# Performance work log

Hardware: AMD Instinct MI355X
Metric: run time of the kernel (lower is better)

Reference implementation:

```python
import jax, jax.numpy as jnp
import numpy as np
from jax import lax

WIDTH = 3.0
SIGMA = 1.0
REDIST_ITERS = 10
B, N = 64, 512  # grid is N x N


def _coords(H, W):
    ys = jnp.arange(H, dtype=jnp.float32)[:, None] * jnp.ones((1, W), jnp.float32)
    xs = jnp.arange(W, dtype=jnp.float32)[None, :] * jnp.ones((H, 1), jnp.float32)
    return xs, ys  # x = column, y = row


def _bilinear_splat(values, xf, yf, H, W):
    """Scatter-add `values` at continuous (xf, yf) with bilinear weights."""
    x0 = jnp.floor(xf)
    y0 = jnp.floor(yf)
    fx = xf - x0
    fy = yf - y0
    x0i = x0.astype(jnp.int32)
    y0i = y0.astype(jnp.int32)
    grid = jnp.zeros((H, W), values.dtype)
    for dx, dy in ((0, 0), (1, 0), (0, 1), (1, 1)):
        xi = x0i + dx
        yi = y0i + dy
        w = (fx if dx else 1.0 - fx) * (fy if dy else 1.0 - fy)
        valid = (xi >= 0) & (xi < W) & (yi >= 0) & (yi < H)
        xi_c = jnp.clip(xi, 0, W - 1)
        yi_c = jnp.clip(yi, 0, H - 1)
        grid = grid.at[yi_c, xi_c].add(jnp.where(valid, w * values, 0.0))
    return grid


def _push_one(rho, p0, p1):
    """Differentiable push via bilinear splat. rho: (H, W) image convention."""
    H, W = rho.shape
    xs, ys = _coords(H, W)
    d = p1 - p0
    L = jnp.sqrt(jnp.sum(d * d) + 1e-12)
    u = d / L                              # unit push direction (x, y)
    n = jnp.stack([-u[1], u[0]])           # unit normal
    rx = xs - p0[0]
    ry = ys - p0[1]
    s = rx * u[0] + ry * u[1]              # along-push coordinate
    t = rx * n[0] + ry * n[1]              # perpendicular coordinate
    sig = jax.nn.sigmoid
    mask = sig((WIDTH - jnp.abs(t)) / SIGMA) * sig(s / SIGMA) * sig((L - s) / SIGMA)
    moved = rho * mask
    disp = jnp.maximum(L - s, 0.0)         # push swept mass to the tool front
    xf = (xs + disp * u[0]).ravel()
    yf = (ys + disp * u[1]).ravel()
    splat = _bilinear_splat(moved.ravel(), xf, yf, H, W)
    return rho * (1.0 - mask) + splat, mask


def _redistribute_one(rho, u):
    """Diffuse occupancy excess (>1) one voxel forward along u, iteratively."""
    H, W = rho.shape
    xs, ys = _coords(H, W)
    xf = (xs + u[0]).ravel()
    yf = (ys + u[1]).ravel()

    def step(r, _):
        exc = jax.nn.relu(r - 1.0)
        shifted = _bilinear_splat(exc.ravel(), xf, yf, H, W)
        return r - exc + shifted, None

    rho, _ = lax.scan(step, rho, None, length=REDIST_ITERS)
    return rho


def setup_inputs() -> dict:
    key = jax.random.key(0)
    k1, k2, k3 = jax.random.split(key, 3)
    occ = jax.random.uniform(k1, (B, N, N), dtype=jnp.float32)
    action_start = jax.random.uniform(k2, (B, 2), dtype=jnp.float32) * (N - 1)
    action_end = jax.random.uniform(k3, (B, 2), dtype=jnp.float32) * (N - 1)
    return {"occ": occ, "action_start": action_start, "action_end": action_end}


def reference(occ, action_start, action_end):
    rho = jnp.transpose(occ, (0, 2, 1))          # (B, Nx, Ny) -> (B, H=y, W=x)
    p0 = action_start[:, :2]
    p1 = action_end[:, :2]
    rho_new, _ = jax.vmap(_push_one)(rho, p0, p1)
    d = p1 - p0
    d_norm = jnp.sqrt(jnp.sum(d * d, axis=-1))
    u = d / jnp.maximum(d_norm, 1e-6)[:, None]
    rho_red = jax.vmap(_redistribute_one)(rho_new, u)
    rho_out = jnp.where((d_norm > 1e-6)[:, None, None], rho_red, rho_new)
    return jnp.transpose(rho_out, (0, 2, 1))
```

## Files before the change

### kernel.cpp

```cpp
#include <hip/hip_runtime.h>

#define NN   512
#define NN2  (NN * NN)
#define BB   64
#define ITERS 10
#define WM   40
#define WWIN (WM * WM)
#define SBLK 16
#define NSPLAT (BB * SBLK)
#define GPT  4
#define NSTREAM 2048
#define FTPB 512

#define RD   64
#define RST  69
#define RTPB 1024

__device__ __forceinline__ float sigf(float x) { return 1.0f / (1.0f + __expf(-x)); }

__device__ __forceinline__ float maskf(float s, float t, float L) {
    if (fabsf(t) > 30.f || s < -30.f || s > L + 30.f) return 0.f;
    return sigf(3.f - fabsf(t)) * sigf(s) * sigf(L - s);
}

__device__ __forceinline__ float base_elem2(float o, float s, float t, float L) {
    float m = maskf(s, t, L);
    return (s >= L) ? o : o * (1.f - m);
}

__global__ void __launch_bounds__(FTPB) fused_kernel(
        const float* __restrict__ occ,
        const float* __restrict__ as_,
        const float* __restrict__ ae_,
        float* __restrict__ ws,
        float* __restrict__ out) {
    __shared__ float win[WWIN];
    const int bid = blockIdx.x;
    const int tid = threadIdx.x;

    if (bid < NSPLAT) {
        const int b  = bid >> 4;
        const int qb = bid & (SBLK - 1);

        const float p0x = as_[2 * b], p0y = as_[2 * b + 1];
        const float p1x = ae_[2 * b], p1y = ae_[2 * b + 1];
        const float dx = p1x - p0x, dy = p1y - p0y;
        const float L  = sqrtf(dx * dx + dy * dy + 1e-12f);
        const float u0 = dx / L, u1 = dy / L;
        const float au0 = fabsf(u0), au1 = fabsf(u1);
        const int wx0 = (int)floorf(p1x - 16.f * au1) - 2;
        const int wy0 = (int)floorf(p1y - 16.f * au0) - 2;
        const bool degen = (dx == 0.f && dy == 0.f);

        for (int k = tid; k < WWIN; k += FTPB) win[k] = 0.f;
        __syncthreads();

        if (!degen) {
            const float* ob = occ + ((size_t)b << 18);
            const bool caseA = (au0 >= au1);
            const int wave = tid >> 6;
            const int lane = tid & 63;

            #pragma unroll
            for (int k2 = 0; k2 < 4; ++k2) {
                const int a = qb + 16 * (wave + 8 * k2);
                const float fa = (float)a;
                float lo, hi;
                bool skip = false;
                if (caseA) {
                    float rxl = fa - p0x;
                    float c1 = p0y + (rxl * u1 - 16.f) / u0;
                    float c2 = p0y + (rxl * u1 + 16.f) / u0;
                    lo = fminf(c1, c2); hi = fmaxf(c1, c2);
                    if (au1 > 1e-6f) {
                        float c3 = p0y + (-16.f - rxl * u0) / u1;
                        float c4 = p0y + (L     - rxl * u0) / u1;
                        lo = fmaxf(lo, fminf(c3, c4));
                        hi = fminf(hi, fmaxf(c3, c4));
                    } else {
                        float sc = rxl * u0;
                        skip = (sc < -16.5f) || (sc > L + 0.5f);
                    }
                } else {
                    float ryl = fa - p0y;
                    float c1 = p0x + (ryl * u0 - 16.f) / u1;
                    float c2 = p0x + (ryl * u0 + 16.f) / u1;
                    lo = fminf(c1, c2); hi = fmaxf(c1, c2);
                    if (au0 > 1e-6f) {
                        float c3 = p0x + (-16.f - ryl * u1) / u0;
                        float c4 = p0x + (L     - ryl * u1) / u0;
                        lo = fmaxf(lo, fminf(c3, c4));
                        hi = fminf(hi, fmaxf(c3, c4));
                    } else {
                        float sc = ryl * u1;
                        skip = (sc < -16.5f) || (sc > L + 0.5f);
                    }
                }
                if (skip) continue;
                int clo = max((int)floorf(lo) - 1, 0);
                int chi = min((int)ceilf(hi) + 1, NN - 1);

                for (int c = clo + lane; c <= chi; c += 64) {
                    int i = caseA ? a : c;
                    int j = caseA ? c : a;
                    float rx = (float)i - p0x, ry = (float)j - p0y;
                    float s = rx * u0 + ry * u1;
                    float t = -rx * u1 + ry * u0;
                    if (fabsf(t) > 16.f || s < -16.f || s >= L) continue;
                    float rho = ob[i * NN + j];
                    float mask  = sigf(3.f - fabsf(t)) * sigf(s) * sigf(L - s);
                    float moved = rho * mask;
                    if (moved <= 1e-10f) continue;
                    float xf = p1x - t * u1;
                    float yf = p1y + t * u0;
                    float x0 = floorf(xf), y0 = floorf(yf);
                    float fx = xf - x0, fy = yf - y0;
                    int base = ((int)x0 - wx0) * WM + ((int)y0 - wy0);
                    atomicAdd(&win[base],          (1.f - fx) * (1.f - fy) * moved);
                    atomicAdd(&win[base + 1],      (1.f - fx) * fy * moved);
                    atomicAdd(&win[base + WM],     fx * (1.f - fy) * moved);
                    atomicAdd(&win[base + WM + 1], fx * fy * moved);
                }
            }
        }
        __syncthreads();
        float* wsb = ws + (size_t)bid * WWIN;
        for (int k = tid; k < WWIN; k += FTPB) wsb[k] = win[k];
    } else {
        const int sb = bid - NSPLAT;
        const int b  = sb >> 5;

        const float p0x = as_[2 * b], p0y = as_[2 * b + 1];
        const float p1x = ae_[2 * b], p1y = ae_[2 * b + 1];
        const float dx = p1x - p0x, dy = p1y - p0y;
        const float L  = sqrtf(dx * dx + dy * dy + 1e-12f);
        const float u0 = dx / L, u1 = dy / L;
        const bool degen = (dx == 0.f && dy == 0.f);

        const float* ob   = occ + ((size_t)b << 18);
        float*       outb = out + ((size_t)b << 18);
        const int rem0 = (sb & 31) * (FTPB * GPT);

        #pragma unroll
        for (int k = 0; k < GPT; ++k) {
            int rem = rem0 + k * FTPB + tid;
            int i   = rem >> 7;
            int j0  = (rem & 127) << 2;
            float4 o4 = *reinterpret_cast<const float4*>(ob + i * NN + j0);
            float4 v;
            float rx = (float)i - p0x;
            float ry = (float)j0 - p0y;
            float s0 = rx * u0 + ry * u1;
            float t0 = -rx * u1 + ry * u0;
            float s3 = s0 + 3.f * u1;
            float t3 = t0 + 3.f * u0;
            float tA = fminf(t0, t3), tB = fmaxf(t0, t3);
            float sA = fminf(s0, s3), sB = fmaxf(s0, s3);
            if (degen || tA > 30.f || tB < -30.f || sB < -30.f || sA >= L) {
                v = o4;
            } else {
                v.x = base_elem2(o4.x, s0,            t0,            L);
                v.y = base_elem2(o4.y, s0 + u1,       t0 + u0,       L);
                v.z = base_elem2(o4.z, s0 + 2.f * u1, t0 + 2.f * u0, L);
                v.w = base_elem2(o4.w, s3,            t3,            L);
            }
            *reinterpret_cast<float4*>(outb + i * NN + j0) = v;
        }
    }
}

__global__ void __launch_bounds__(RTPB) redist_kernel(
        const float* __restrict__ ws,
        const float* __restrict__ as_,
        const float* __restrict__ ae_,
        float* __restrict__ out) {
    __shared__ float smem[RD * RST];
    __shared__ float winsum[WWIN];
    const int b   = blockIdx.x;
    const int tid = threadIdx.x;

    const float p0x = as_[2 * b], p0y = as_[2 * b + 1];
    const float p1x = ae_[2 * b], p1y = ae_[2 * b + 1];
    const float dx = p1x - p0x, dy = p1y - p0y;
    const float L  = sqrtf(dx * dx + dy * dy + 1e-12f);
    const float pu0 = dx / L, pu1 = dy / L;
    const float au0 = fabsf(pu0), au1 = fabsf(pu1);
    const int wx0 = (int)floorf(p1x - 16.f * au1) - 2;
    const int wy0 = (int)floorf(p1y - 16.f * au0) - 2;
    const int rx0 = wx0 - 12;
    const int ry0 = wy0 - 12;
    const float dn  = sqrtf(dx * dx + dy * dy);
    const bool active = dn > 1e-6f;
    const float rdn = fmaxf(dn, 1e-6f);
    const float ru0 = dx / rdn, ru1 = dy / rdn;
    const float s0f = floorf(ru0), s1f = floorf(ru1);
    const float f0 = ru0 - s0f, f1 = ru1 - s1f;
    const int oi = -(int)s0f;
    const int oj = -(int)s1f;
    const float wA0 = 1.f - f0, wB0 = f0;
    const float wA1 = 1.f - f1, wB1 = f1;

    const float* wsb  = ws  + (size_t)b * (SBLK * WWIN);
    float*       outb = out + ((size_t)b << 18);

    for (int k = tid; k < WWIN; k += RTPB) {
        float s = 0.f;
        #pragma unroll
        for (int w = 0; w < SBLK; ++w) s += wsb[w * WWIN + k];
        winsum[k] = s;
    }
    __syncthreads();

    const int li = tid >> 4;
    const int lj = (tid & 15) << 2;
    const int gi = rx0 + li;
    const int gj = ry0 + lj;
    const bool rok = (gi >= 0) && (gi < NN);
    float4 vm, r = make_float4(0.f, 0.f, 0.f, 0.f);
    vm.x = (rok && (unsigned)(gj + 0) < NN) ? 1.f : 0.f;
    vm.y = (rok && (unsigned)(gj + 1) < NN) ? 1.f : 0.f;
    vm.z = (rok && (unsigned)(gj + 2) < NN) ? 1.f : 0.f;
    vm.w = (rok && (unsigned)(gj + 3) < NN) ? 1.f : 0.f;
    if (rok) {
        const float* orow = outb + gi * NN;
        int cx = li - 12;
        bool cxok = (unsigned)cx < (unsigned)WM;
        float* rp = (float*)&r;
        const float* vmp = (const float*)&vm;
        #pragma unroll
        for (int e = 0; e < 4; ++e) {
            if (vmp[e] > 0.f) {
                float t = orow[gj + e];
                int cy = lj + e - 12;
                if (cxok && (unsigned)cy < (unsigned)WM) t += winsum[cx * WM + cy];
                rp[e] = t;
            }
        }
    }

    const int rA  = min(max(li + oi, 0), RD - 1);
    const int dB  = (min(max(li + oi - 1, 0), RD - 1) - rA) * RST;
    const int wa  = li * RST + lj;
    const int aA0 = rA * RST + max(lj + oj - 1, 0);
    const int aA1 = rA * RST + (lj + oj + 0);
    const int aA2 = rA * RST + (lj + oj + 1);
    const int aA3 = rA * RST + (lj + oj + 2);
    const int aA4 = rA * RST + min(lj + oj + 3, RD - 1);

    if (active) {
        for (int it = 0; it < ITERS; ++it) {
            smem[wa + 0] = fmaxf(r.x - 1.f, 0.f);
            smem[wa + 1] = fmaxf(r.y - 1.f, 0.f);
            smem[wa + 2] = fmaxf(r.z - 1.f, 0.f);
            smem[wa + 3] = fmaxf(r.w - 1.f, 0.f);
            __syncthreads();
            float eA0 = smem[aA0], eA1 = smem[aA1], eA2 = smem[aA2];
            float eA3 = smem[aA3], eA4 = smem[aA4];
            float eB0 = smem[aA0 + dB], eB1 = smem[aA1 + dB];
            float eB2 = smem[aA2 + dB], eB3 = smem[aA3 + dB];
            float eB4 = smem[aA4 + dB];
            float g;
            g = wA0 * (wA1 * eA1 + wB1 * eA0) + wB0 * (wA1 * eB1 + wB1 * eB0);
            r.x = (fminf(r.x, 1.f) + g) * vm.x;
            g = wA0 * (wA1 * eA2 + wB1 * eA1) + wB0 * (wA1 * eB2 + wB1 * eB1);
            r.y = (fminf(r.y, 1.f) + g) * vm.y;
            g = wA0 * (wA1 * eA3 + wB1 * eA2) + wB0 * (wA1 * eB3 + wB1 * eB2);
            r.z = (fminf(r.z, 1.f) + g) * vm.z;
            g = wA0 * (wA1 * eA4 + wB1 * eA3) + wB0 * (wA1 * eB4 + wB1 * eB3);
            r.w = (fminf(r.w, 1.f) + g) * vm.w;
            __syncthreads();
        }
    }

    if (rok) {
        float* orow = outb + gi * NN;
        if (vm.x > 0.f) orow[gj + 0] = r.x;
        if (vm.y > 0.f) orow[gj + 1] = r.y;
        if (vm.z > 0.f) orow[gj + 2] = r.z;
        if (vm.w > 0.f) orow[gj + 3] = r.w;
    }
}

extern "C" void kernel_launch(void* const* d_in, const int* in_sizes, int n_in,
                              void* d_out, int out_size, void* d_ws, size_t ws_size,
                              hipStream_t stream) {
    const float* occ = (const float*)d_in[0];
    const float* as_ = (const float*)d_in[1];
    const float* ae_ = (const float*)d_in[2];
    float* out = (float*)d_out;
    float* ws  = (float*)d_ws;

    fused_kernel<<<NSPLAT + NSTREAM, FTPB, 0, stream>>>(occ, as_, ae_, ws, out);

    redist_kernel<<<BB, RTPB, 0, stream>>>(ws, as_, ae_, out);
}
```

Baseline: 51.89 us.

## Interleave splat and stream blocks, hoist loads, use nontemporal loads/stores

Changes the block-to-role mapping so every third block does splat work and the other two stream, spreading the heavier splat blocks across the grid instead of launching them all first. The streaming path now issues all four float4 loads up front before computing, and uses nontemporal loads and stores to avoid polluting cache. The aim is better load balance across CUs and more memory-level parallelism. The risk is that nontemporal stores make the later redist kernel's reads of out miss in cache.

```diff
diff --git a/kernel.cpp b/kernel.cpp
--- a/kernel.cpp
+++ b/kernel.cpp
@@ -10,11 +10,14 @@
 #define NSPLAT (BB * SBLK)
 #define GPT  4
 #define NSTREAM 2048
+#define NBLK (NSPLAT + NSTREAM)
 #define FTPB 512
 
 #define RD   64
 #define RST  69
 #define RTPB 1024
+
+typedef float floatx4 __attribute__((ext_vector_type(4)));
 
 __device__ __forceinline__ float sigf(float x) { return 1.0f / (1.0f + __expf(-x)); }
 
@@ -37,10 +40,12 @@
     __shared__ float win[WWIN];
     const int bid = blockIdx.x;
     const int tid = threadIdx.x;
-
-    if (bid < NSPLAT) {
-        const int b  = bid >> 4;
-        const int qb = bid & (SBLK - 1);
+    const int q   = bid / 3;
+    const int r   = bid - 3 * q;
+
+    if (r == 2) {
+        const int b  = q >> 4;
+        const int qb = q & (SBLK - 1);
 
         const float p0x = as_[2 * b], p0y = as_[2 * b + 1];
         const float p1x = ae_[2 * b], p1y = ae_[2 * b + 1];
@@ -124,10 +129,10 @@
             }
         }
         __syncthreads();
-        float* wsb = ws + (size_t)bid * WWIN;
+        float* wsb = ws + (size_t)q * WWIN;
         for (int k = tid; k < WWIN; k += FTPB) wsb[k] = win[k];
     } else {
-        const int sb = bid - NSPLAT;
+        const int sb = 2 * q + r;
         const int b  = sb >> 5;
 
         const float p0x = as_[2 * b], p0y = as_[2 * b + 1];
@@ -139,33 +144,55 @@
 
         const float* ob   = occ + ((size_t)b << 18);
         float*       outb = out + ((size_t)b << 18);
-        const int rem0 = (sb & 31) * (FTPB * GPT);
-
-        #pragma unroll
-        for (int k = 0; k < GPT; ++k) {
-            int rem = rem0 + k * FTPB + tid;
-            int i   = rem >> 7;
-            int j0  = (rem & 127) << 2;
-            float4 o4 = *reinterpret_cast<const float4*>(ob + i * NN + j0);
-            float4 v;
-            float rx = (float)i - p0x;
-            float ry = (float)j0 - p0y;
-            float s0 = rx * u0 + ry * u1;
-            float t0 = -rx * u1 + ry * u0;
-            float s3 = s0 + 3.f * u1;
-            float t3 = t0 + 3.f * u0;
-            float tA = fminf(t0, t3), tB = fmaxf(t0, t3);
-            float sA = fminf(s0, s3), sB = fmaxf(s0, s3);
-            if (degen || tA > 30.f || tB < -30.f || sB < -30.f || sA >= L) {
-                v = o4;
-            } else {
-                v.x = base_elem2(o4.x, s0,            t0,            L);
-                v.y = base_elem2(o4.y, s0 + u1,       t0 + u0,       L);
-                v.z = base_elem2(o4.z, s0 + 2.f * u1, t0 + 2.f * u0, L);
-                v.w = base_elem2(o4.w, s3,            t3,            L);
-            }
-            *reinterpret_cast<float4*>(outb + i * NN + j0) = v;
-        }
+        const int rem0 = (sb & 31) * (FTPB * GPT) + tid;
+
+        floatx4 o0, o1, o2, o3;
+        {
+            int rem, i, j0;
+            rem = rem0;             i = rem >> 7; j0 = (rem & 127) << 2;
+            o0 = __builtin_nontemporal_load(
+                     reinterpret_cast<const floatx4*>(ob + i * NN + j0));
+            rem = rem0 + FTPB;      i = rem >> 7; j0 = (rem & 127) << 2;
+            o1 = __builtin_nontemporal_load(
+                     reinterpret_cast<const floatx4*>(ob + i * NN + j0));
+            rem = rem0 + 2 * FTPB;  i = rem >> 7; j0 = (rem & 127) << 2;
+            o2 = __builtin_nontemporal_load(
+                     reinterpret_cast<const floatx4*>(ob + i * NN + j0));
+            rem = rem0 + 3 * FTPB;  i = rem >> 7; j0 = (rem & 127) << 2;
+            o3 = __builtin_nontemporal_load(
+                     reinterpret_cast<const floatx4*>(ob + i * NN + j0));
+        }
+
+        #define STREAM_ONE(KK, OV)                                               \
+        {                                                                        \
+            int rem = rem0 + (KK) * FTPB;                                        \
+            int i   = rem >> 7;                                                  \
+            int j0  = (rem & 127) << 2;                                          \
+            floatx4 v;                                                           \
+            float rx = (float)i - p0x;                                           \
+            float ry = (float)j0 - p0y;                                          \
+            float s0 = rx * u0 + ry * u1;                                        \
+            float t0 = -rx * u1 + ry * u0;                                       \
+            float s3 = s0 + 3.f * u1;                                            \
+            float t3 = t0 + 3.f * u0;                                            \
+            float tA = fminf(t0, t3), tB = fmaxf(t0, t3);                        \
+            float sA = fminf(s0, s3), sB = fmaxf(s0, s3);                        \
+            if (degen || tA > 30.f || tB < -30.f || sB < -30.f || sA >= L) {     \
+                v = OV;                                                          \
+            } else {                                                             \
+                v.x = base_elem2(OV.x, s0,            t0,            L);         \
+                v.y = base_elem2(OV.y, s0 + u1,       t0 + u0,       L);         \
+                v.z = base_elem2(OV.z, s0 + 2.f * u1, t0 + 2.f * u0, L);         \
+                v.w = base_elem2(OV.w, s3,            t3,            L);         \
+            }                                                                    \
+            __builtin_nontemporal_store(v,                                       \
+                reinterpret_cast<floatx4*>(outb + i * NN + j0));                 \
+        }
+        STREAM_ONE(0, o0)
+        STREAM_ONE(1, o1)
+        STREAM_ONE(2, o2)
+        STREAM_ONE(3, o3)
+        #undef STREAM_ONE
     }
 }
 
@@ -290,7 +317,7 @@
     float* out = (float*)d_out;
     float* ws  = (float*)d_ws;
 
-    fused_kernel<<<NSPLAT + NSTREAM, FTPB, 0, stream>>>(occ, as_, ae_, ws, out);
+    fused_kernel<<<NBLK, FTPB, 0, stream>>>(occ, as_, ae_, ws, out);
 
     redist_kernel<<<BB, RTPB, 0, stream>>>(ws, as_, ae_, out);
 }
```

Result: faster. 49.58 us (-4.5%).
